# Performance work log

Measured on AMD Instinct MI355X. Metric: run time of the kernel, lower is better.

## Reference

```python
import jax, jax.numpy as jnp
import numpy as np

NEG = -1.0e30  # finite stand-in for -inf (NaN-safe under autodiff)


def rnnt_loss_mean(logits, ys, ylen):
    # logits: (B, T, U+1, V); ys: (B, U) int labels; ylen: (B,) label lengths.
    # blank index = 0; per the original forward, xlen == T for every batch element.
    lp = jax.nn.log_softmax(logits, axis=-1)
    lp_blank = lp[..., 0]  # (B, T, U1)
    # lp_label[b, t, u] = lp[b, t, u, ys[b, u]]  for u < U
    lp_label = jnp.take_along_axis(
        lp[:, :, :-1, :], ys[:, None, :, None].astype(jnp.int32), axis=3
    )[..., 0]  # (B, T, U)
    B, T, U1 = lp_blank.shape
    # emit[b, t, u] = lp_label[b, t, u-1], with emit[..., 0] = -inf
    emit = jnp.concatenate([jnp.full((B, T, 1), NEG, lp.dtype), lp_label], axis=2)
    # alpha[0, u] = sum_{k<u} lp_label[b, 0, k]
    row0 = jnp.concatenate(
        [jnp.zeros((B, 1), lp.dtype), jnp.cumsum(lp_label[:, 0, :], axis=1)], axis=1
    )  # (B, U1)

    def u_step(carry, au_eu):
        a_u, e_u = au_eu  # each (B,)
        new = jnp.logaddexp(a_u, carry + e_u)
        return new, new

    def t_step(prev_row, inp):
        blank_prev, emit_t = inp  # each (B, U1)
        a = prev_row + blank_prev  # horizontal (time) move
        init = jnp.full((B,), NEG, lp.dtype)
        _, new_row = jax.lax.scan(u_step, init, (a.T, emit_t.T))  # (U1, B)
        return new_row.T, None

    last_row, _ = jax.lax.scan(
        t_step,
        row0,
        (jnp.swapaxes(lp_blank[:, :-1, :], 0, 1), jnp.swapaxes(emit[:, 1:, :], 0, 1)),
    )  # (B, U1) = alpha[T-1, :]
    yl = ylen[:, None].astype(jnp.int32)
    alpha_end = jnp.take_along_axis(last_row, yl, axis=1)[:, 0]
    blank_end = jnp.take_along_axis(lp_blank[:, T - 1, :], yl, axis=1)[:, 0]
    return jnp.mean(-(alpha_end + blank_end))


def setup_inputs():
    B, T, U, H, V = 8, 200, 50, 320, 1024
    key = jax.random.key(0)
    ks = jax.random.split(key, 12)
    s = np.float32(1.0 / np.sqrt(H))
    return {
        "encoder_output": jax.random.normal(ks[0], (B, T, H), jnp.float32),
        "prediction_output": jax.random.normal(ks[1], (B, U + 1, H), jnp.float32),
        "xs": jax.random.normal(ks[2], (B, T, 80), jnp.float32),  # unused by forward
        "xlen": jnp.full((B,), T, jnp.int32),  # overwritten to T in original code
        "ys": jax.random.randint(ks[3], (B, U), 1, V, dtype=jnp.int32),
        "ylen": jax.random.randint(ks[4], (B,), 1, U + 1, dtype=jnp.int32),
        "W_enc": jax.random.normal(ks[5], (H, H), jnp.float32) * s,
        "b_enc": jnp.zeros((H,), jnp.float32),
        "W_pred": jax.random.normal(ks[6], (H, H), jnp.float32) * s,
        "b_pred": jnp.zeros((H,), jnp.float32),
        "W_ff_enc": jax.random.normal(ks[7], (H, V), jnp.float32) * s,
        "W_ff_pred": jax.random.normal(ks[8], (H, V), jnp.float32) * s,
        "b_ff": jnp.zeros((V,), jnp.float32),
    }


def reference(encoder_output, prediction_output, xs, xlen, ys, ylen,
              W_enc, b_enc, W_pred, b_pred, W_ff_enc, W_ff_pred, b_ff):
    # linear_enc / linear_pred commute with the broadcast-expand, so apply them first.
    enc_proj = encoder_output @ W_enc + b_enc        # (B, T, H)
    pred_proj = prediction_output @ W_pred + b_pred  # (B, U1, H)
    # cat + linear_feed_forward == split-weight matmuls summed over the broadcast.
    enc_part = enc_proj @ W_ff_enc    # (B, T, V)
    pred_part = pred_proj @ W_ff_pred  # (B, U1, V)
    logits = enc_part[:, :, None, :] + pred_part[:, None, :, :] + b_ff  # (B, T, U1, V)
    loss = rnnt_loss_mean(logits, ys, ylen)
    return loss, logits
```

## Files before the change

### kernel.cpp

```cpp
#include <hip/hip_runtime.h>
#include <hip/hip_bf16.h>
#include <cstddef>

#define Bdim 8
#define Tdim 200
#define Udim 50
#define U1dim 51
#define Hdim 320
#define Vdim 1024
#define NEGV -1.0e30f

using short8 = __attribute__((ext_vector_type(8))) short;
using f32x4  = __attribute__((ext_vector_type(4))) float;

static __device__ __forceinline__ ushort f2bf(float x) {
    __hip_bfloat16 h = __float2bfloat16(x);
    return *reinterpret_cast<ushort*>(&h);
}
static __device__ __forceinline__ int pack2(float a, float b) {
    return (int)f2bf(a) | ((int)f2bf(b) << 16);
}

__global__ __launch_bounds__(256) void fuse_weights(
    const float* __restrict__ W_enc, const float* __restrict__ W_ff_enc,
    const float* __restrict__ W_pred, const float* __restrict__ W_ff_pred,
    const float* __restrict__ b_enc, const float* __restrict__ b_pred,
    const float* __restrict__ b_ff,
    ushort* __restrict__ Wfe_t, ushort* __restrict__ Wfp_t,
    float* __restrict__ cvec, float* __restrict__ dvec)
{
    const int tid = threadIdx.x;
    if (blockIdx.y == 16) {
        if (blockIdx.x > 1) return;
        const bool e = (blockIdx.x == 0);
        const float* bv = e ? b_enc : b_pred;
        const float* Wf = e ? W_ff_enc : W_ff_pred;
        float* ovec = e ? cvec : dvec;
        const int v = tid * 4;
        float4 acc = make_float4(0.f, 0.f, 0.f, 0.f);
        for (int p = 0; p < Hdim; ++p) {
            float s = bv[p];
            float4 w = *(const float4*)&Wf[(size_t)p * Vdim + v];
            acc.x += s * w.x; acc.y += s * w.y; acc.z += s * w.z; acc.w += s * w.w;
        }
        if (e) {
            float4 bf = *(const float4*)&b_ff[v];
            acc.x += bf.x; acc.y += bf.y; acc.z += bf.z; acc.w += bf.w;
        }
        *(float4*)&ovec[v] = acc;
        return;
    }

    const bool e = (blockIdx.x < 5);
    const float* A  = e ? W_ff_enc : W_ff_pred;
    const float* Bm = e ? W_enc    : W_pred;
    ushort* Cout    = e ? Wfe_t    : Wfp_t;
    const int n0 = (blockIdx.x % 5) * 64;
    const int m0 = blockIdx.y * 64;

    __shared__ short As[64][40];
    __shared__ short Bs[64][40];

    const int ar = tid >> 3;
    const int ac = (tid & 7) * 8;
    const int br = tid >> 2;
    const int bc = (tid & 3) * 8;

    const int lane = tid & 63;
    const int wave = tid >> 6;
    const int wr = wave >> 1, wc = wave & 1;
    const int lrow = lane & 15;
    const int kg = (lane >> 4) * 8;

    f32x4 acc[2][2] = {};

    for (int k0 = 0; k0 < Hdim; k0 += 32) {
        float4 a0 = *(const float4*)&A[(size_t)(k0 + ar) * Vdim + m0 + ac];
        float4 a1 = *(const float4*)&A[(size_t)(k0 + ar) * Vdim + m0 + ac + 4];
        As[ac + 0][ar] = (short)f2bf(a0.x);
        As[ac + 1][ar] = (short)f2bf(a0.y);
        As[ac + 2][ar] = (short)f2bf(a0.z);
        As[ac + 3][ar] = (short)f2bf(a0.w);
        As[ac + 4][ar] = (short)f2bf(a1.x);
        As[ac + 5][ar] = (short)f2bf(a1.y);
        As[ac + 6][ar] = (short)f2bf(a1.z);
        As[ac + 7][ar] = (short)f2bf(a1.w);
        float4 w0 = *(const float4*)&Bm[(size_t)(n0 + br) * Hdim + k0 + bc];
        float4 w1 = *(const float4*)&Bm[(size_t)(n0 + br) * Hdim + k0 + bc + 4];
        int4 bp = make_int4(pack2(w0.x, w0.y), pack2(w0.z, w0.w),
                            pack2(w1.x, w1.y), pack2(w1.z, w1.w));
        *(int4*)&Bs[br][bc] = bp;
        __syncthreads();

        short8 fa0 = *(const short8*)&As[wr * 32 + lrow][kg];
        short8 fa1 = *(const short8*)&As[wr * 32 + 16 + lrow][kg];
        short8 fb0 = *(const short8*)&Bs[wc * 32 + lrow][kg];
        short8 fb1 = *(const short8*)&Bs[wc * 32 + 16 + lrow][kg];
        acc[0][0] = __builtin_amdgcn_mfma_f32_16x16x32_bf16(fa0, fb0, acc[0][0], 0, 0, 0);
        acc[0][1] = __builtin_amdgcn_mfma_f32_16x16x32_bf16(fa0, fb1, acc[0][1], 0, 0, 0);
        acc[1][0] = __builtin_amdgcn_mfma_f32_16x16x32_bf16(fa1, fb0, acc[1][0], 0, 0, 0);
        acc[1][1] = __builtin_amdgcn_mfma_f32_16x16x32_bf16(fa1, fb1, acc[1][1], 0, 0, 0);
        __syncthreads();
    }

    #pragma unroll
    for (int fm = 0; fm < 2; ++fm) {
        #pragma unroll
        for (int fn = 0; fn < 2; ++fn) {
            int col = n0 + wc * 32 + fn * 16 + lrow;
            int r0 = m0 + wr * 32 + fm * 16 + (lane >> 4) * 4;
            #pragma unroll
            for (int r = 0; r < 4; ++r)
                Cout[(size_t)(r0 + r) * Hdim + col] = f2bf(acc[fm][fn][r]);
        }
    }
}

__global__ __launch_bounds__(256) void main_gemm(
    const float* __restrict__ enc, const float* __restrict__ pred,
    const ushort* __restrict__ Wfe_t, const ushort* __restrict__ Wfp_t,
    const float* __restrict__ cvec, const float* __restrict__ dvec,
    float* __restrict__ enc_part, float* __restrict__ pred_part)
{
    const bool e = (blockIdx.y < 25);
    const float*  A    = e ? enc : pred;
    const ushort* Bt   = e ? Wfe_t : Wfp_t;
    const float*  bias = e ? cvec : dvec;
    float*        C    = e ? enc_part : pred_part;
    const int M  = e ? (Bdim * Tdim) : (Bdim * U1dim);
    const int m0 = (e ? blockIdx.y : blockIdx.y - 25) * 64;
    const int n0 = blockIdx.x * 64;

    __shared__ short As[64][40];
    __shared__ short Bs[64][40];
    const int tid = threadIdx.x;
    const int sr = tid >> 2;
    const int sc = (tid & 3) * 8;

    const int lane = tid & 63;
    const int wave = tid >> 6;
    const int wr = wave >> 1, wc = wave & 1;
    const int lrow = lane & 15;
    const int kg = (lane >> 4) * 8;

    f32x4 acc[2][2] = {};

    for (int k0 = 0; k0 < Hdim; k0 += 32) {
        int4 av = make_int4(0, 0, 0, 0);
        if (m0 + sr < M) {
            float4 x0 = *(const float4*)&A[(size_t)(m0 + sr) * Hdim + k0 + sc];
            float4 x1 = *(const float4*)&A[(size_t)(m0 + sr) * Hdim + k0 + sc + 4];
            av = make_int4(pack2(x0.x, x0.y), pack2(x0.z, x0.w),
                           pack2(x1.x, x1.y), pack2(x1.z, x1.w));
        }
        *(int4*)&As[sr][sc] = av;
        *(int4*)&Bs[sr][sc] = *(const int4*)&Bt[(size_t)(n0 + sr) * Hdim + k0 + sc];
        __syncthreads();

        short8 fa0 = *(const short8*)&As[wr * 32 + lrow][kg];
        short8 fa1 = *(const short8*)&As[wr * 32 + 16 + lrow][kg];
        short8 fb0 = *(const short8*)&Bs[wc * 32 + lrow][kg];
        short8 fb1 = *(const short8*)&Bs[wc * 32 + 16 + lrow][kg];
        acc[0][0] = __builtin_amdgcn_mfma_f32_16x16x32_bf16(fa0, fb0, acc[0][0], 0, 0, 0);
        acc[0][1] = __builtin_amdgcn_mfma_f32_16x16x32_bf16(fa0, fb1, acc[0][1], 0, 0, 0);
        acc[1][0] = __builtin_amdgcn_mfma_f32_16x16x32_bf16(fa1, fb0, acc[1][0], 0, 0, 0);
        acc[1][1] = __builtin_amdgcn_mfma_f32_16x16x32_bf16(fa1, fb1, acc[1][1], 0, 0, 0);
        __syncthreads();
    }

    #pragma unroll
    for (int fm = 0; fm < 2; ++fm) {
        #pragma unroll
        for (int fn = 0; fn < 2; ++fn) {
            int col = n0 + wc * 32 + fn * 16 + lrow;
            int r0 = m0 + wr * 32 + fm * 16 + (lane >> 4) * 4;
            float bv = bias[col];
            #pragma unroll
            for (int r = 0; r < 4; ++r) {
                int row = r0 + r;
                if (row < M)
                    C[(size_t)row * Vdim + col] = acc[fm][fn][r] + bv;
            }
        }
    }
}

__global__ __launch_bounds__(256) void joint_lse(
    const float* __restrict__ enc_part, const float* __restrict__ pred_part,
    const int* __restrict__ ys, float* __restrict__ out,
    float* __restrict__ lp_blank, float* __restrict__ lp_label)
{
    const int bt = blockIdx.x;
    const int b = bt / Tdim;
    const int tid = threadIdx.x;
    const int lane = tid & 63;
    const int wave = tid >> 6;
    if (bt == 0 && tid == 0) out[0] = 0.f;

    const float* Erow = enc_part + (size_t)bt * Vdim + lane * 16;
    float4 e0 = *(const float4*)(Erow + 0);
    float4 e1 = *(const float4*)(Erow + 4);
    float4 e2 = *(const float4*)(Erow + 8);
    float4 e3 = *(const float4*)(Erow + 12);

    const float* Pbase = pred_part + (size_t)b * U1dim * Vdim + lane * 16;
    float* region = out + 1 + (size_t)bt * U1dim * Vdim;

    int u = wave;
    float4 p0, p1, p2, p3;
    {
        const float* P = Pbase + (size_t)u * Vdim;
        p0 = *(const float4*)(P + 0);
        p1 = *(const float4*)(P + 4);
        p2 = *(const float4*)(P + 8);
        p3 = *(const float4*)(P + 12);
    }

    for (; u < U1dim; u += 4) {
        float4 q0, q1, q2, q3;
        const int un = u + 4;
        if (un < U1dim) {
            const float* P = Pbase + (size_t)un * Vdim;
            q0 = *(const float4*)(P + 0);
            q1 = *(const float4*)(P + 4);
            q2 = *(const float4*)(P + 8);
            q3 = *(const float4*)(P + 12);
        }

        float xa[16];
        xa[0]=e0.x+p0.x;  xa[1]=e0.y+p0.y;  xa[2]=e0.z+p0.z;  xa[3]=e0.w+p0.w;
        xa[4]=e1.x+p1.x;  xa[5]=e1.y+p1.y;  xa[6]=e1.z+p1.z;  xa[7]=e1.w+p1.w;
        xa[8]=e2.x+p2.x;  xa[9]=e2.y+p2.y;  xa[10]=e2.z+p2.z; xa[11]=e2.w+p2.w;
        xa[12]=e3.x+p3.x; xa[13]=e3.y+p3.y; xa[14]=e3.z+p3.z; xa[15]=e3.w+p3.w;

        float nx0 = __shfl_down(xa[0], 1);
        float nx1 = __shfl_down(xa[1], 1);
        float nx2 = __shfl_down(xa[2], 1);

        float* rowb = region + (size_t)u * Vdim;
        float* W = rowb + 3 + lane * 16;
        *(float4*)(W + 0) = make_float4(xa[3],  xa[4],  xa[5],  xa[6]);
        *(float4*)(W + 4) = make_float4(xa[7],  xa[8],  xa[9],  xa[10]);
        *(float4*)(W + 8) = make_float4(xa[11], xa[12], xa[13], xa[14]);
        if (lane < 63) {
            *(float4*)(W + 12) = make_float4(xa[15], nx0, nx1, nx2);
        } else {
            rowb[1023] = xa[15];
        }
        if (lane == 0) {
            rowb[0] = xa[0];
            rowb[1] = xa[1];
            rowb[2] = xa[2];
        }

        float s = 0.f;
        #pragma unroll
        for (int i = 0; i < 16; ++i) s += __expf(xa[i]);
        #pragma unroll
        for (int off = 32; off >= 1; off >>= 1) s += __shfl_xor(s, off);
        float lse = __logf(s);

        int vlab = (u < Udim) ? ys[b * Udim + u] : 0;
        int idx = vlab & 15;
        int src = vlab >> 4;
        float cand = xa[0];
        #pragma unroll
        for (int i = 1; i < 16; ++i) if (i == idx) cand = xa[i];
        float lab = __shfl(cand, src);

        if (lane == 0) {
            lp_blank[(size_t)bt * U1dim + u] = xa[0] - lse;
            if (u < Udim) lp_label[(size_t)bt * Udim + u] = lab - lse;
        }

        p0 = q0; p1 = q1; p2 = q2; p3 = q3;
    }
}

__global__ __launch_bounds__(256) void alpha_kernel(
    const float* __restrict__ lp_blank, const float* __restrict__ lp_label,
    const int* __restrict__ ylen, float* __restrict__ out)
{
    __shared__ float s_bl[U1dim * Tdim];
    __shared__ float s_lab[Udim * Tdim];
    const int b = blockIdx.x;
    const int tid = threadIdx.x;
    const float* gb = lp_blank + (size_t)b * Tdim * U1dim;
    const float* gl = lp_label + (size_t)b * Tdim * Udim;
    for (int i = tid; i < Tdim * U1dim; i += 256) {
        int t = i / U1dim, u = i % U1dim;
        s_bl[u * Tdim + t] = gb[i];
    }
    for (int i = tid; i < Tdim * Udim; i += 256) {
        int t = i / Udim, u = i % Udim;
        s_lab[u * Tdim + t] = gl[i];
    }
    __syncthreads();

    if (tid < 64) {
        const int u = tid;
        float cur = NEGV;
        for (int d = 0; d < Tdim + U1dim - 1; ++d) {
            float left = __shfl_up(cur, 1);
            int t = d - u;
            if (u < U1dim && t >= 0 && t < Tdim) {
                float h = (t >= 1) ? cur + s_bl[u * Tdim + (t - 1)] : NEGV;
                float g = (u >= 1) ? left + s_lab[(u - 1) * Tdim + t] : NEGV;
                float mx = fmaxf(h, g);
                float nv = mx + log1pf(__expf(-fabsf(h - g)));
                if (d == 0) nv = 0.f;
                cur = nv;
            }
        }
        const int L = ylen[b];
        if (u == L)
            atomicAdd(out, -(cur + s_bl[L * Tdim + (Tdim - 1)]) * (1.0f / Bdim));
    }
}

extern "C" void kernel_launch(void* const* d_in, const int* in_sizes, int n_in,
                              void* d_out, int out_size, void* d_ws, size_t ws_size,
                              hipStream_t stream)
{
    const float* enc      = (const float*)d_in[0];
    const float* pred     = (const float*)d_in[1];
    const int*   ys       = (const int*)d_in[4];
    const int*   ylen     = (const int*)d_in[5];
    const float* W_enc    = (const float*)d_in[6];
    const float* b_enc    = (const float*)d_in[7];
    const float* W_pred   = (const float*)d_in[8];
    const float* b_pred   = (const float*)d_in[9];
    const float* W_ff_enc = (const float*)d_in[10];
    const float* W_ff_pred= (const float*)d_in[11];
    const float* b_ff     = (const float*)d_in[12];
    float* out = (float*)d_out;
    char* ws = (char*)d_ws;

    float*  enc_part  = (float*) (ws + 0);
    float*  pred_part = (float*) (ws + 6553600);
    ushort* Wfe_t     = (ushort*)(ws + 8224768);
    ushort* Wfp_t     = (ushort*)(ws + 8880128);
    float*  cvec      = (float*) (ws + 9535488);
    float*  dvec      = (float*) (ws + 9539584);
    float*  lp_blank  = (float*) (ws + 9543680);
    float*  lp_label  = (float*) (ws + 9870080);

    dim3 blk(256);
    fuse_weights<<<dim3(10, 17), blk, 0, stream>>>(
        W_enc, W_ff_enc, W_pred, W_ff_pred, b_enc, b_pred, b_ff,
        Wfe_t, Wfp_t, cvec, dvec);
    main_gemm<<<dim3(16, 32), blk, 0, stream>>>(
        enc, pred, Wfe_t, Wfp_t, cvec, dvec, enc_part, pred_part);
    joint_lse<<<dim3(Bdim * Tdim), blk, 0, stream>>>(
        enc_part, pred_part, ys, out, lp_blank, lp_label);
    alpha_kernel<<<dim3(Bdim), blk, 0, stream>>>(lp_blank, lp_label, ylen, out);
}
```

Measured before the change: 246.0 us.

## Retile joint kernel for pred-row reuse across time steps; use base-2 logaddexp

The joint/log-softmax kernel now has each wave handle four time steps and loop over all label positions, so each pred_part row it loads is reused across four enc rows. The grid shrinks from 1600 blocks to 104 blocks (8x13), and the last chunk leaves some waves idle. The alpha recursion is moved into the base-2 domain, using exp2/log2 with scaled inputs instead of expf/log1pf. The retiling cuts pred_part reloads but greatly lowers parallelism for a kernel dominated by logits stores, which may hurt the achievable write bandwidth.

```diff
diff --git a/kernel.cpp b/kernel.cpp
--- a/kernel.cpp
+++ b/kernel.cpp
@@ -9,6 +9,8 @@
 #define Hdim 320
 #define Vdim 1024
 #define NEGV -1.0e30f
+#define LOG2E 1.4426950408889634f
+#define LN2f  0.6931471805599453f
 
 using short8 = __attribute__((ext_vector_type(8))) short;
 using f32x4  = __attribute__((ext_vector_type(4))) float;
@@ -190,87 +192,100 @@
     const int* __restrict__ ys, float* __restrict__ out,
     float* __restrict__ lp_blank, float* __restrict__ lp_label)
 {
-    const int bt = blockIdx.x;
-    const int b = bt / Tdim;
+    const int b = blockIdx.x;
+    const int chunk = blockIdx.y;
     const int tid = threadIdx.x;
     const int lane = tid & 63;
     const int wave = tid >> 6;
-    if (bt == 0 && tid == 0) out[0] = 0.f;
-
-    const float* Erow = enc_part + (size_t)bt * Vdim + lane * 16;
-    float4 e0 = *(const float4*)(Erow + 0);
-    float4 e1 = *(const float4*)(Erow + 4);
-    float4 e2 = *(const float4*)(Erow + 8);
-    float4 e3 = *(const float4*)(Erow + 12);
+    if (b == 0 && chunk == 0 && tid == 0) out[0] = 0.f;
+    const int t0 = chunk * 16 + wave * 4;
+    if (t0 >= Tdim) return;
+
+    float4 e0[4], e1[4], e2[4], e3[4];
+    #pragma unroll
+    for (int j = 0; j < 4; ++j) {
+        const float* Erow = enc_part + (size_t)(b * Tdim + t0 + j) * Vdim + lane * 16;
+        e0[j] = *(const float4*)(Erow + 0);
+        e1[j] = *(const float4*)(Erow + 4);
+        e2[j] = *(const float4*)(Erow + 8);
+        e3[j] = *(const float4*)(Erow + 12);
+    }
 
     const float* Pbase = pred_part + (size_t)b * U1dim * Vdim + lane * 16;
-    float* region = out + 1 + (size_t)bt * U1dim * Vdim;
-
-    int u = wave;
+    float* logits = out + 1;
+
     float4 p0, p1, p2, p3;
     {
-        const float* P = Pbase + (size_t)u * Vdim;
+        const float* P = Pbase;
         p0 = *(const float4*)(P + 0);
         p1 = *(const float4*)(P + 4);
         p2 = *(const float4*)(P + 8);
         p3 = *(const float4*)(P + 12);
     }
 
-    for (; u < U1dim; u += 4) {
+    for (int u = 0; u < U1dim; ++u) {
         float4 q0, q1, q2, q3;
-        const int un = u + 4;
-        if (un < U1dim) {
-            const float* P = Pbase + (size_t)un * Vdim;
+        if (u + 1 < U1dim) {
+            const float* P = Pbase + (size_t)(u + 1) * Vdim;
             q0 = *(const float4*)(P + 0);
             q1 = *(const float4*)(P + 4);
             q2 = *(const float4*)(P + 8);
             q3 = *(const float4*)(P + 12);
         }
 
-        float xa[16];
-        xa[0]=e0.x+p0.x;  xa[1]=e0.y+p0.y;  xa[2]=e0.z+p0.z;  xa[3]=e0.w+p0.w;
-        xa[4]=e1.x+p1.x;  xa[5]=e1.y+p1.y;  xa[6]=e1.z+p1.z;  xa[7]=e1.w+p1.w;
-        xa[8]=e2.x+p2.x;  xa[9]=e2.y+p2.y;  xa[10]=e2.z+p2.z; xa[11]=e2.w+p2.w;
-        xa[12]=e3.x+p3.x; xa[13]=e3.y+p3.y; xa[14]=e3.z+p3.z; xa[15]=e3.w+p3.w;
-
-        float nx0 = __shfl_down(xa[0], 1);
-        float nx1 = __shfl_down(xa[1], 1);
-        float nx2 = __shfl_down(xa[2], 1);
-
-        float* rowb = region + (size_t)u * Vdim;
-        float* W = rowb + 3 + lane * 16;
-        *(float4*)(W + 0) = make_float4(xa[3],  xa[4],  xa[5],  xa[6]);
-        *(float4*)(W + 4) = make_float4(xa[7],  xa[8],  xa[9],  xa[10]);
-        *(float4*)(W + 8) = make_float4(xa[11], xa[12], xa[13], xa[14]);
-        if (lane < 63) {
-            *(float4*)(W + 12) = make_float4(xa[15], nx0, nx1, nx2);
-        } else {
-            rowb[1023] = xa[15];
-        }
-        if (lane == 0) {
-            rowb[0] = xa[0];
-            rowb[1] = xa[1];
-            rowb[2] = xa[2];
-        }
-
-        float s = 0.f;
+        const int vlab = (u < Udim) ? ys[b * Udim + u] : 0;
+        const int idx = vlab & 15;
+        const int src = vlab >> 4;
+
         #pragma unroll
-        for (int i = 0; i < 16; ++i) s += __expf(xa[i]);
-        #pragma unroll
-        for (int off = 32; off >= 1; off >>= 1) s += __shfl_xor(s, off);
-        float lse = __logf(s);
-
-        int vlab = (u < Udim) ? ys[b * Udim + u] : 0;
-        int idx = vlab & 15;
-        int src = vlab >> 4;
-        float cand = xa[0];
-        #pragma unroll
-        for (int i = 1; i < 16; ++i) if (i == idx) cand = xa[i];
-        float lab = __shfl(cand, src);
-
-        if (lane == 0) {
-            lp_blank[(size_t)bt * U1dim + u] = xa[0] - lse;
-            if (u < Udim) lp_label[(size_t)bt * Udim + u] = lab - lse;
+        for (int j = 0; j < 4; ++j) {
+            float xa[16];
+            xa[0] = e0[j].x + p0.x;  xa[1] = e0[j].y + p0.y;
+            xa[2] = e0[j].z + p0.z;  xa[3] = e0[j].w + p0.w;
+            xa[4] = e1[j].x + p1.x;  xa[5] = e1[j].y + p1.y;
+            xa[6] = e1[j].z + p1.z;  xa[7] = e1[j].w + p1.w;
+            xa[8] = e2[j].x + p2.x;  xa[9] = e2[j].y + p2.y;
+            xa[10]= e2[j].z + p2.z;  xa[11]= e2[j].w + p2.w;
+            xa[12]= e3[j].x + p3.x;  xa[13]= e3[j].y + p3.y;
+            xa[14]= e3[j].z + p3.z;  xa[15]= e3[j].w + p3.w;
+
+            float nx0 = __shfl_down(xa[0], 1);
+            float nx1 = __shfl_down(xa[1], 1);
+            float nx2 = __shfl_down(xa[2], 1);
+
+            const int bt = b * Tdim + t0 + j;
+            float* rowb = logits + ((size_t)bt * U1dim + u) * Vdim;
+            float* W = rowb + 3 + lane * 16;
+            *(float4*)(W + 0) = make_float4(xa[3],  xa[4],  xa[5],  xa[6]);
+            *(float4*)(W + 4) = make_float4(xa[7],  xa[8],  xa[9],  xa[10]);
+            *(float4*)(W + 8) = make_float4(xa[11], xa[12], xa[13], xa[14]);
+            if (lane < 63) {
+                *(float4*)(W + 12) = make_float4(xa[15], nx0, nx1, nx2);
+            } else {
+                rowb[1023] = xa[15];
+            }
+            if (lane == 0) {
+                rowb[0] = xa[0];
+                rowb[1] = xa[1];
+                rowb[2] = xa[2];
+            }
+
+            float s = 0.f;
+            #pragma unroll
+            for (int i = 0; i < 16; ++i) s += __expf(xa[i]);
+            #pragma unroll
+            for (int off = 32; off >= 1; off >>= 1) s += __shfl_xor(s, off);
+            float lse = __logf(s);
+
+            float cand = xa[0];
+            #pragma unroll
+            for (int i = 1; i < 16; ++i) if (i == idx) cand = xa[i];
+            float lab = __shfl(cand, src);
+
+            if (lane == 0) {
+                lp_blank[(size_t)bt * U1dim + u] = xa[0] - lse;
+                if (u < Udim) lp_label[(size_t)bt * Udim + u] = lab - lse;
+            }
         }
 
         p0 = q0; p1 = q1; p2 = q2; p3 = q3;
@@ -289,11 +304,11 @@
     const float* gl = lp_label + (size_t)b * Tdim * Udim;
     for (int i = tid; i < Tdim * U1dim; i += 256) {
         int t = i / U1dim, u = i % U1dim;
-        s_bl[u * Tdim + t] = gb[i];
+        s_bl[u * Tdim + t] = gb[i] * LOG2E;
     }
     for (int i = tid; i < Tdim * Udim; i += 256) {
         int t = i / Udim, u = i % Udim;
-        s_lab[u * Tdim + t] = gl[i];
+        s_lab[u * Tdim + t] = gl[i] * LOG2E;
     }
     __syncthreads();
 
@@ -307,14 +322,14 @@
                 float h = (t >= 1) ? cur + s_bl[u * Tdim + (t - 1)] : NEGV;
                 float g = (u >= 1) ? left + s_lab[(u - 1) * Tdim + t] : NEGV;
                 float mx = fmaxf(h, g);
-                float nv = mx + log1pf(__expf(-fabsf(h - g)));
+                float nv = mx + __log2f(1.0f + exp2f(-fabsf(h - g)));
                 if (d == 0) nv = 0.f;
                 cur = nv;
             }
         }
         const int L = ylen[b];
         if (u == L)
-            atomicAdd(out, -(cur + s_bl[L * Tdim + (Tdim - 1)]) * (1.0f / Bdim));
+            atomicAdd(out, -(cur + s_bl[L * Tdim + (Tdim - 1)]) * (LN2f / Bdim));
     }
 }
 
@@ -351,7 +366,7 @@
         Wfe_t, Wfp_t, cvec, dvec);
     main_gemm<<<dim3(16, 32), blk, 0, stream>>>(
         enc, pred, Wfe_t, Wfp_t, cvec, dvec, enc_part, pred_part);
-    joint_lse<<<dim3(Bdim * Tdim), blk, 0, stream>>>(
+    joint_lse<<<dim3(Bdim, 13), blk, 0, stream>>>(
         enc_part, pred_part, ys, out, lp_blank, lp_label);
     alpha_kernel<<<dim3(Bdim), blk, 0, stream>>>(lp_blank, lp_label, ylen, out);
 }
```

New measurement: 222.8 us. -9.4%, faster.

## Share pred rows via LDS across eight time steps in joint_lse

Applied to the files above, without the earlier changes.

joint_lse now has each 512-thread block handle eight time steps of one batch element. Blocks stage pred_part rows into shared memory in chunks of 13 rows with a permuted layout, so each pred row is read from global memory once per block instead of once per time step. The bias-vector computation moves out of fuse_weights into a separate 1024-thread kernel. The alpha recursion switches to base-2 exp/log on prescaled inputs. The cost is an extra kernel launch, more LDS use and barriers, and lower occupancy for the joint kernel. That kernel is likely dominated by the large logits store anyway.

```diff
diff --git a/kernel.cpp b/kernel.cpp
--- a/kernel.cpp
+++ b/kernel.cpp
@@ -9,6 +9,8 @@
 #define Hdim 320
 #define Vdim 1024
 #define NEGV -1.0e30f
+#define LOG2E 1.4426950408889634f
+#define LN2f  0.6931471805599453f
 
 using short8 = __attribute__((ext_vector_type(8))) short;
 using f32x4  = __attribute__((ext_vector_type(4))) float;
@@ -24,33 +26,9 @@
 __global__ __launch_bounds__(256) void fuse_weights(
     const float* __restrict__ W_enc, const float* __restrict__ W_ff_enc,
     const float* __restrict__ W_pred, const float* __restrict__ W_ff_pred,
-    const float* __restrict__ b_enc, const float* __restrict__ b_pred,
-    const float* __restrict__ b_ff,
-    ushort* __restrict__ Wfe_t, ushort* __restrict__ Wfp_t,
-    float* __restrict__ cvec, float* __restrict__ dvec)
+    ushort* __restrict__ Wfe_t, ushort* __restrict__ Wfp_t)
 {
     const int tid = threadIdx.x;
-    if (blockIdx.y == 16) {
-        if (blockIdx.x > 1) return;
-        const bool e = (blockIdx.x == 0);
-        const float* bv = e ? b_enc : b_pred;
-        const float* Wf = e ? W_ff_enc : W_ff_pred;
-        float* ovec = e ? cvec : dvec;
-        const int v = tid * 4;
-        float4 acc = make_float4(0.f, 0.f, 0.f, 0.f);
-        for (int p = 0; p < Hdim; ++p) {
-            float s = bv[p];
-            float4 w = *(const float4*)&Wf[(size_t)p * Vdim + v];
-            acc.x += s * w.x; acc.y += s * w.y; acc.z += s * w.z; acc.w += s * w.w;
-        }
-        if (e) {
-            float4 bf = *(const float4*)&b_ff[v];
-            acc.x += bf.x; acc.y += bf.y; acc.z += bf.z; acc.w += bf.w;
-        }
-        *(float4*)&ovec[v] = acc;
-        return;
-    }
-
     const bool e = (blockIdx.x < 5);
     const float* A  = e ? W_ff_enc : W_ff_pred;
     const float* Bm = e ? W_enc    : W_pred;
@@ -116,6 +94,25 @@
     }
 }
 
+__global__ __launch_bounds__(1024) void bias_vec(
+    const float* __restrict__ b_enc, const float* __restrict__ W_ff_enc,
+    const float* __restrict__ b_pred, const float* __restrict__ W_ff_pred,
+    const float* __restrict__ b_ff,
+    float* __restrict__ cvec, float* __restrict__ dvec)
+{
+    const bool e = (blockIdx.x == 0);
+    const float* bv = e ? b_enc : b_pred;
+    const float* Wf = e ? W_ff_enc : W_ff_pred;
+    float* ovec = e ? cvec : dvec;
+    const int v = threadIdx.x;
+    float acc = 0.f;
+    #pragma unroll 8
+    for (int p = 0; p < Hdim; ++p)
+        acc += bv[p] * Wf[(size_t)p * Vdim + v];
+    if (e) acc += b_ff[v];
+    ovec[v] = acc;
+}
+
 __global__ __launch_bounds__(256) void main_gemm(
     const float* __restrict__ enc, const float* __restrict__ pred,
     const ushort* __restrict__ Wfe_t, const ushort* __restrict__ Wfp_t,
@@ -185,17 +182,21 @@
     }
 }
 
-__global__ __launch_bounds__(256) void joint_lse(
+#define CHUNK 13
+__global__ __launch_bounds__(512) void joint_lse(
     const float* __restrict__ enc_part, const float* __restrict__ pred_part,
     const int* __restrict__ ys, float* __restrict__ out,
     float* __restrict__ lp_blank, float* __restrict__ lp_label)
 {
-    const int bt = blockIdx.x;
-    const int b = bt / Tdim;
+    __shared__ float S[CHUNK * Vdim];
+    const int b = blockIdx.x;
+    const int oct = blockIdx.y;
     const int tid = threadIdx.x;
     const int lane = tid & 63;
     const int wave = tid >> 6;
-    if (bt == 0 && tid == 0) out[0] = 0.f;
+    const int t = oct * 8 + wave;
+    const int bt = b * Tdim + t;
+    if (b == 0 && oct == 0 && tid == 0) out[0] = 0.f;
 
     const float* Erow = enc_part + (size_t)bt * Vdim + lane * 16;
     float4 e0 = *(const float4*)(Erow + 0);
@@ -203,77 +204,76 @@
     float4 e2 = *(const float4*)(Erow + 8);
     float4 e3 = *(const float4*)(Erow + 12);
 
-    const float* Pbase = pred_part + (size_t)b * U1dim * Vdim + lane * 16;
+    const float* Pb = pred_part + (size_t)b * U1dim * Vdim;
     float* region = out + 1 + (size_t)bt * U1dim * Vdim;
 
-    int u = wave;
-    float4 p0, p1, p2, p3;
-    {
-        const float* P = Pbase + (size_t)u * Vdim;
-        p0 = *(const float4*)(P + 0);
-        p1 = *(const float4*)(P + 4);
-        p2 = *(const float4*)(P + 8);
-        p3 = *(const float4*)(P + 12);
-    }
-
-    for (; u < U1dim; u += 4) {
-        float4 q0, q1, q2, q3;
-        const int un = u + 4;
-        if (un < U1dim) {
-            const float* P = Pbase + (size_t)un * Vdim;
-            q0 = *(const float4*)(P + 0);
-            q1 = *(const float4*)(P + 4);
-            q2 = *(const float4*)(P + 8);
-            q3 = *(const float4*)(P + 12);
-        }
-
-        float xa[16];
-        xa[0]=e0.x+p0.x;  xa[1]=e0.y+p0.y;  xa[2]=e0.z+p0.z;  xa[3]=e0.w+p0.w;
-        xa[4]=e1.x+p1.x;  xa[5]=e1.y+p1.y;  xa[6]=e1.z+p1.z;  xa[7]=e1.w+p1.w;
-        xa[8]=e2.x+p2.x;  xa[9]=e2.y+p2.y;  xa[10]=e2.z+p2.z; xa[11]=e2.w+p2.w;
-        xa[12]=e3.x+p3.x; xa[13]=e3.y+p3.y; xa[14]=e3.z+p3.z; xa[15]=e3.w+p3.w;
-
-        float nx0 = __shfl_down(xa[0], 1);
-        float nx1 = __shfl_down(xa[1], 1);
-        float nx2 = __shfl_down(xa[2], 1);
-
-        float* rowb = region + (size_t)u * Vdim;
-        float* W = rowb + 3 + lane * 16;
-        *(float4*)(W + 0) = make_float4(xa[3],  xa[4],  xa[5],  xa[6]);
-        *(float4*)(W + 4) = make_float4(xa[7],  xa[8],  xa[9],  xa[10]);
-        *(float4*)(W + 8) = make_float4(xa[11], xa[12], xa[13], xa[14]);
-        if (lane < 63) {
-            *(float4*)(W + 12) = make_float4(xa[15], nx0, nx1, nx2);
-        } else {
-            rowb[1023] = xa[15];
-        }
-        if (lane == 0) {
-            rowb[0] = xa[0];
-            rowb[1] = xa[1];
-            rowb[2] = xa[2];
-        }
-
-        float s = 0.f;
-        #pragma unroll
-        for (int i = 0; i < 16; ++i) s += __expf(xa[i]);
-        #pragma unroll
-        for (int off = 32; off >= 1; off >>= 1) s += __shfl_xor(s, off);
-        float lse = __logf(s);
-
-        int vlab = (u < Udim) ? ys[b * Udim + u] : 0;
-        int idx = vlab & 15;
-        int src = vlab >> 4;
-        float cand = xa[0];
-        #pragma unroll
-        for (int i = 1; i < 16; ++i) if (i == idx) cand = xa[i];
-        float lab = __shfl(cand, src);
-
-        if (lane == 0) {
-            lp_blank[(size_t)bt * U1dim + u] = xa[0] - lse;
-            if (u < Udim) lp_label[(size_t)bt * Udim + u] = lab - lse;
-        }
-
-        p0 = q0; p1 = q1; p2 = q2; p3 = q3;
+    for (int c = 0; c < 4; ++c) {
+        const int u0 = c * CHUNK;
+        const int rows = (u0 + CHUNK <= U1dim) ? CHUNK : (U1dim - u0);
+        const int nf4 = rows * 256;
+        __syncthreads();
+        for (int idx = tid; idx < nf4; idx += 512) {
+            const int ul = idx >> 8;
+            const int j  = idx & 255;
+            float4 vv = *(const float4*)&Pb[(size_t)(u0 + ul) * Vdim + j * 4];
+            *(float4*)&S[ul * Vdim + ((j & 3) * 64 + (j >> 2)) * 4] = vv;
+        }
+        __syncthreads();
+
+        for (int ul = 0; ul < rows; ++ul) {
+            const int u = u0 + ul;
+            const float* Sr = &S[ul * Vdim];
+            float4 p0 = *(const float4*)&Sr[(0 * 64 + lane) * 4];
+            float4 p1 = *(const float4*)&Sr[(1 * 64 + lane) * 4];
+            float4 p2 = *(const float4*)&Sr[(2 * 64 + lane) * 4];
+            float4 p3 = *(const float4*)&Sr[(3 * 64 + lane) * 4];
+
+            float xa[16];
+            xa[0]=e0.x+p0.x;  xa[1]=e0.y+p0.y;  xa[2]=e0.z+p0.z;  xa[3]=e0.w+p0.w;
+            xa[4]=e1.x+p1.x;  xa[5]=e1.y+p1.y;  xa[6]=e1.z+p1.z;  xa[7]=e1.w+p1.w;
+            xa[8]=e2.x+p2.x;  xa[9]=e2.y+p2.y;  xa[10]=e2.z+p2.z; xa[11]=e2.w+p2.w;
+            xa[12]=e3.x+p3.x; xa[13]=e3.y+p3.y; xa[14]=e3.z+p3.z; xa[15]=e3.w+p3.w;
+
+            float nx0 = __shfl_down(xa[0], 1);
+            float nx1 = __shfl_down(xa[1], 1);
+            float nx2 = __shfl_down(xa[2], 1);
+
+            float* rowb = region + (size_t)u * Vdim;
+            float* W = rowb + 3 + lane * 16;
+            *(float4*)(W + 0) = make_float4(xa[3],  xa[4],  xa[5],  xa[6]);
+            *(float4*)(W + 4) = make_float4(xa[7],  xa[8],  xa[9],  xa[10]);
+            *(float4*)(W + 8) = make_float4(xa[11], xa[12], xa[13], xa[14]);
+            if (lane < 63) {
+                *(float4*)(W + 12) = make_float4(xa[15], nx0, nx1, nx2);
+            } else {
+                rowb[1023] = xa[15];
+            }
+            if (lane == 0) {
+                rowb[0] = xa[0];
+                rowb[1] = xa[1];
+                rowb[2] = xa[2];
+            }
+
+            float s = 0.f;
+            #pragma unroll
+            for (int i = 0; i < 16; ++i) s += __expf(xa[i]);
+            #pragma unroll
+            for (int off = 32; off >= 1; off >>= 1) s += __shfl_xor(s, off);
+            float lse = __logf(s);
+
+            const int vlab = (u < Udim) ? ys[b * Udim + u] : 0;
+            const int idx = vlab & 15;
+            const int src = vlab >> 4;
+            float cand = xa[0];
+            #pragma unroll
+            for (int i = 1; i < 16; ++i) if (i == idx) cand = xa[i];
+            float lab = __shfl(cand, src);
+
+            if (lane == 0) {
+                lp_blank[(size_t)bt * U1dim + u] = xa[0] - lse;
+                if (u < Udim) lp_label[(size_t)bt * Udim + u] = lab - lse;
+            }
+        }
     }
 }
 
@@ -289,11 +289,11 @@
     const float* gl = lp_label + (size_t)b * Tdim * Udim;
     for (int i = tid; i < Tdim * U1dim; i += 256) {
         int t = i / U1dim, u = i % U1dim;
-        s_bl[u * Tdim + t] = gb[i];
+        s_bl[u * Tdim + t] = gb[i] * LOG2E;
     }
     for (int i = tid; i < Tdim * Udim; i += 256) {
         int t = i / Udim, u = i % Udim;
-        s_lab[u * Tdim + t] = gl[i];
+        s_lab[u * Tdim + t] = gl[i] * LOG2E;
     }
     __syncthreads();
 
@@ -307,14 +307,14 @@
                 float h = (t >= 1) ? cur + s_bl[u * Tdim + (t - 1)] : NEGV;
                 float g = (u >= 1) ? left + s_lab[(u - 1) * Tdim + t] : NEGV;
                 float mx = fmaxf(h, g);
-                float nv = mx + log1pf(__expf(-fabsf(h - g)));
+                float nv = mx + __log2f(1.0f + exp2f(-fabsf(h - g)));
                 if (d == 0) nv = 0.f;
                 cur = nv;
             }
         }
         const int L = ylen[b];
         if (u == L)
-            atomicAdd(out, -(cur + s_bl[L * Tdim + (Tdim - 1)]) * (1.0f / Bdim));
+            atomicAdd(out, -(cur + s_bl[L * Tdim + (Tdim - 1)]) * (LN2f / Bdim));
     }
 }
 
@@ -345,13 +345,14 @@
     float*  lp_blank  = (float*) (ws + 9543680);
     float*  lp_label  = (float*) (ws + 9870080);
 
-    dim3 blk(256);
-    fuse_weights<<<dim3(10, 17), blk, 0, stream>>>(
-        W_enc, W_ff_enc, W_pred, W_ff_pred, b_enc, b_pred, b_ff,
-        Wfe_t, Wfp_t, cvec, dvec);
-    main_gemm<<<dim3(16, 32), blk, 0, stream>>>(
+    fuse_weights<<<dim3(10, 16), dim3(256), 0, stream>>>(
+        W_enc, W_ff_enc, W_pred, W_ff_pred, Wfe_t, Wfp_t);
+    bias_vec<<<dim3(2), dim3(1024), 0, stream>>>(
+        b_enc, W_ff_enc, b_pred, W_ff_pred, b_ff, cvec, dvec);
+    main_gemm<<<dim3(16, 32), dim3(256), 0, stream>>>(
         enc, pred, Wfe_t, Wfp_t, cvec, dvec, enc_part, pred_part);
-    joint_lse<<<dim3(Bdim * Tdim), blk, 0, stream>>>(
+    joint_lse<<<dim3(Bdim, 25), dim3(512), 0, stream>>>(
         enc_part, pred_part, ys, out, lp_blank, lp_label);
-    alpha_kernel<<<dim3(Bdim), blk, 0, stream>>>(lp_blank, lp_label, ylen, out);
-}
+    alpha_kernel<<<dim3(Bdim), dim3(256), 0, stream>>>(
+        lp_blank, lp_label, ylen, out);
+}
```

New measurement: 201.2 us. 18.2% less time.
